# Kernel tuning notes

Hardware: AMD Instinct MI355X
Metric: run time of the kernel (lower is better)

Reference implementation:

```python
import jax, jax.numpy as jnp
import numpy as np
from jax import lax

NPRE = 900        # num_proposal_pre (hardcoded in module)
NPOST = 64        # num_proposal init arg
MAXV = 8          # max vertices of intersection of two convex quads
NMS_THRESH = 0.85
BN_EPS = 1e-5


def boxes3d_to_bev(b):
    # b: (N,7) = (x,y,z,h,w,l,ry) -> BEV rotated box (x1,y1,x2,y2,ry) on x-z plane
    cu, cv = b[:, 0], b[:, 2]
    half_l, half_w = b[:, 5] * 0.5, b[:, 4] * 0.5
    return jnp.stack([cu - half_l, cv - half_w, cu + half_l, cv + half_w, b[:, 6]], axis=-1)


def rect_corners(bev):
    # bev: (N,5) -> (N,4,2) CCW corners of rotated rect
    cx = (bev[:, 0] + bev[:, 2]) * 0.5
    cy = (bev[:, 1] + bev[:, 3]) * 0.5
    hx = (bev[:, 2] - bev[:, 0]) * 0.5
    hy = (bev[:, 3] - bev[:, 1]) * 0.5
    c, s = jnp.cos(bev[:, 4]), jnp.sin(bev[:, 4])
    lx = jnp.stack([-hx, hx, hx, -hx], -1)   # (N,4)
    ly = jnp.stack([-hy, -hy, hy, hy], -1)
    X = cx[:, None] + c[:, None] * lx - s[:, None] * ly
    Y = cy[:, None] + s[:, None] * lx + c[:, None] * ly
    return jnp.stack([X, Y], -1)


def _clip(poly, cnt, a, b):
    # Sutherland-Hodgman clip of poly (MAXV,2) with cnt valid verts by half-plane
    # left of directed edge a->b (clip quad is CCW).
    n = b - a
    def side(p):
        return n[0] * (p[1] - a[1]) - n[1] * (p[0] - a[0])
    out = jnp.zeros_like(poly)
    ocnt = jnp.int32(0)
    for i in range(MAXV):
        valid = i < cnt
        cur = poly[i]
        nxt = poly[jnp.where(i + 1 < cnt, i + 1, 0)]
        dc, dn = side(cur), side(nxt)
        in_c, in_n = dc >= 0, dn >= 0
        e1 = valid & in_c
        out = jnp.where(e1, out.at[ocnt].set(cur), out)
        ocnt = ocnt + e1.astype(jnp.int32)
        e2 = valid & (in_c != in_n)
        denom = dc - dn
        t = dc / jnp.where(denom == 0, 1.0, denom)
        ip = cur + t * (nxt - cur)
        out = jnp.where(e2, out.at[ocnt].set(ip), out)
        ocnt = ocnt + e2.astype(jnp.int32)
    return out, ocnt


def _pair_inter(ca, cb):
    # intersection area of two convex quads given CCW corners (4,2)
    poly = jnp.concatenate([ca, jnp.zeros((MAXV - 4, 2), ca.dtype)], 0)
    cnt = jnp.int32(4)
    for k in range(4):
        poly, cnt = _clip(poly, cnt, cb[k], cb[(k + 1) % 4])
    s = jnp.float32(0.0)
    for i in range(MAXV):
        valid = (i < cnt) & (cnt >= 3)
        j = jnp.where(i + 1 < cnt, i + 1, 0)
        s = s + jnp.where(valid, poly[i, 0] * poly[j, 1] - poly[j, 0] * poly[i, 1], 0.0)
    return jnp.abs(s) * 0.5


def pairwise_iou(corners, areas):
    # row-blocked to keep memory small: lax.map over rows, vmap over cols
    def row(args):
        ci, ai = args
        inter = jax.vmap(lambda cj: _pair_inter(ci, cj))(corners)
        return inter / jnp.maximum(ai + areas - inter, 1e-8)
    return lax.map(row, (corners, areas))


def nms_keep(iou):
    N = iou.shape[0]
    idx = jnp.arange(N)
    def body(i, keep):
        sup = keep[i] & (iou[i] > NMS_THRESH) & (idx > i)
        return keep & (~sup)
    return lax.fori_loop(0, N, body, jnp.ones((N,), bool))


def _forward(search_xyz, search_feature, estimation_cla, template_box,
             W1, b1, gamma, beta, run_mean, run_var, W2, b2):
    B, N = search_xyz.shape[0], search_xyz.shape[1]
    # reg head: conv1d(256->128,k1) + BN(eval) + ReLU + dropout(eval=id) + conv1d(128->4,k1)
    h = jnp.einsum('oi,bin->bon', W1, search_feature) + b1[None, :, None]
    inv = gamma / jnp.sqrt(run_var + BN_EPS)
    h = h * inv[None, :, None] + (beta - run_mean * inv)[None, :, None]
    h = jax.nn.relu(h)
    offset = jnp.einsum('oi,bin->bon', W2, h) + b2[None, :, None]  # (B,4,N)
    offset = jnp.transpose(offset, (0, 2, 1))                       # (B,N,4)
    vote_xyz = search_xyz + offset[..., 0:3]
    tmpl = jnp.broadcast_to(template_box, (B, N, 7))
    proposals = jnp.concatenate([vote_xyz, tmpl[..., 3:6], offset[..., 3:4]], -1)  # (B,N,7)
    scores = jax.nn.sigmoid(estimation_cla[..., 0])  # (B,N)

    def per_batch(sc, pr):
        order = jnp.argsort(-sc)
        s = sc[order[:NPRE]]
        p = pr[order[:NPRE]]
        bev = boxes3d_to_bev(p)
        corners = rect_corners(bev)
        areas = (bev[:, 2] - bev[:, 0]) * (bev[:, 3] - bev[:, 1])
        iou = pairwise_iou(lax.stop_gradient(corners), lax.stop_gradient(areas))
        keep = nms_keep(iou)
        rank = jnp.cumsum(keep.astype(jnp.int32)) - 1
        tgt = jnp.where(keep & (rank < NPOST), rank, NPOST)  # NPOST = dummy slot
        out_b = jnp.zeros((NPOST + 1, 7), p.dtype).at[tgt].set(p)[:NPOST]
        out_s = jnp.zeros((NPOST + 1,), s.dtype).at[tgt].set(s)[:NPOST]
        return out_b, out_s

    ret_bbox3d, ret_scores = jax.vmap(per_batch)(scores, proposals)
    center_xyzs = ret_bbox3d[..., 0:3]
    prop_out = jnp.take(proposals, jnp.array([0, 1, 2, 6]), axis=-1)
    return ret_bbox3d, ret_scores, prop_out, center_xyzs


def setup_inputs():
    key = jax.random.key(0)
    ks = jax.random.split(key, 8)
    B, N, C, H = 8, 16384, 256, 128
    search_xyz = jax.random.normal(ks[0], (B, N, 3), jnp.float32) * 2.0
    search_feature = jax.random.normal(ks[1], (B, C, N), jnp.float32)
    estimation_cla = jax.random.normal(ks[2], (B, N, 1), jnp.float32)
    center = jax.random.normal(ks[3], (B, 1, 3), jnp.float32)
    dims = jax.random.uniform(ks[4], (B, 1, 3), jnp.float32, 1.0, 3.0)
    ry = jax.random.uniform(ks[5], (B, 1, 1), jnp.float32, -np.pi, np.pi)
    template_box = jnp.concatenate([center, dims, ry], -1)
    W1 = jax.random.normal(ks[6], (H, C), jnp.float32) * (1.0 / np.sqrt(C))
    b1 = jnp.zeros((H,), jnp.float32)
    gamma = jnp.ones((H,), jnp.float32)
    beta = jnp.zeros((H,), jnp.float32)
    run_mean = jnp.zeros((H,), jnp.float32)
    run_var = jnp.ones((H,), jnp.float32)
    W2 = jax.random.normal(ks[7], (4, H), jnp.float32) * (1.0 / np.sqrt(H))
    b2 = jnp.zeros((4,), jnp.float32)
    return dict(search_xyz=search_xyz, search_feature=search_feature,
                estimation_cla=estimation_cla, template_box=template_box,
                W1=W1, b1=b1, gamma=gamma, beta=beta,
                run_mean=run_mean, run_var=run_var, W2=W2, b2=b2)


def reference(search_xyz, search_feature, estimation_cla, template_box,
              W1, b1, gamma, beta, run_mean, run_var, W2, b2):
    return _forward(search_xyz, search_feature, estimation_cla, template_box,
                    W1, b1, gamma, beta, run_mean, run_var, W2, b2)
```

## Files before the change

kernel.cpp:

```cpp
#include <hip/hip_runtime.h>
#include <cmath>

#define NTOT 16384
#define NBATCH 8
#define NPRE 900
#define NPOST 64

__global__ __launch_bounds__(256) void mlp_kernel(
    const float* __restrict__ feat, const float* __restrict__ xyz,
    const float* __restrict__ W1, const float* __restrict__ b1,
    const float* __restrict__ gamma, const float* __restrict__ beta,
    const float* __restrict__ rmean, const float* __restrict__ rvar,
    const float* __restrict__ W2, const float* __restrict__ b2,
    float* __restrict__ prop) {
  __shared__ float As[64][128];
  __shared__ float Bs[64][128];
  const int b  = blockIdx.y;
  const int n0 = blockIdx.x * 128;
  const int tid = threadIdx.x;
  const int tr = tid >> 4, tc = tid & 15;
  const float* fb = feat + (size_t)b * 256 * NTOT;

  float acc[8][8];
#pragma unroll
  for (int r = 0; r < 8; ++r)
#pragma unroll
    for (int c = 0; c < 8; ++c) acc[r][c] = 0.f;

  for (int kt = 0; kt < 4; ++kt) {
    {
      const int m = tid & 127, qh = tid >> 7;
#pragma unroll
      for (int p = 0; p < 8; ++p) {
        const int q = qh + p * 2;
        const float4 w = *(const float4*)(W1 + (size_t)m * 256 + kt * 64 + q * 4);
        As[q * 4 + 0][m] = w.x; As[q * 4 + 1][m] = w.y;
        As[q * 4 + 2][m] = w.z; As[q * 4 + 3][m] = w.w;
      }
      const int qq = tid & 31, r0 = tid >> 5;
#pragma unroll
      for (int p = 0; p < 8; ++p) {
        const int k = r0 + p * 8;
        *(float4*)(&Bs[k][qq * 4]) =
            *(const float4*)(fb + (size_t)(kt * 64 + k) * NTOT + n0 + qq * 4);
      }
    }
    __syncthreads();
#pragma unroll 8
    for (int k = 0; k < 64; ++k) {
      float a[8], bb[8];
      *(float4*)&a[0]  = *(const float4*)&As[k][tr * 8];
      *(float4*)&a[4]  = *(const float4*)&As[k][tr * 8 + 4];
      *(float4*)&bb[0] = *(const float4*)&Bs[k][tc * 4];
      *(float4*)&bb[4] = *(const float4*)&Bs[k][64 + tc * 4];
#pragma unroll
      for (int r = 0; r < 8; ++r)
#pragma unroll
        for (int c = 0; c < 8; ++c) acc[r][c] = fmaf(a[r], bb[c], acc[r][c]);
    }
    __syncthreads();
  }

  float po[4][8];
#pragma unroll
  for (int kk = 0; kk < 4; ++kk)
#pragma unroll
    for (int c = 0; c < 8; ++c) po[kk][c] = 0.f;
#pragma unroll
  for (int r = 0; r < 8; ++r) {
    const int row = tr * 8 + r;
    const float inv = gamma[row] / sqrtf(rvar[row] + 1e-5f);
    const float sh  = beta[row] - rmean[row] * inv;
    const float bb1 = b1[row];
    float w2v[4];
#pragma unroll
    for (int kk = 0; kk < 4; ++kk) w2v[kk] = W2[kk * 128 + row];
#pragma unroll
    for (int c = 0; c < 8; ++c) {
      float h = (acc[r][c] + bb1) * inv + sh;
      h = fmaxf(h, 0.f);
#pragma unroll
      for (int kk = 0; kk < 4; ++kk) po[kk][c] += w2v[kk] * h;
    }
  }
  float* po_lds = &As[0][0];
#pragma unroll
  for (int kk = 0; kk < 4; ++kk)
#pragma unroll
    for (int c = 0; c < 8; ++c) {
      const int col = (c < 4) ? (tc * 4 + c) : (64 + tc * 4 + (c - 4));
      po_lds[((tr * 4 + kk) * 128) + col] = po[kk][c];
    }
  __syncthreads();
  float* off_lds = &Bs[0][0];
#pragma unroll
  for (int it = 0; it < 2; ++it) {
    const int idx = tid + it * 256;
    const int kk = idx >> 7, col = idx & 127;
    float sum = b2[kk];
#pragma unroll
    for (int t2 = 0; t2 < 16; ++t2) sum += po_lds[((t2 * 4 + kk) * 128) + col];
    off_lds[kk * 128 + col] = sum;
  }
  __syncthreads();
  if (tid < 128) {
    const int n = n0 + tid;
    const float* sx = xyz + ((size_t)b * NTOT + n) * 3;
    float4 o;
    o.x = sx[0] + off_lds[0 * 128 + tid];
    o.y = sx[1] + off_lds[1 * 128 + tid];
    o.z = sx[2] + off_lds[2 * 128 + tid];
    o.w = off_lds[3 * 128 + tid];
    *(float4*)(prop + ((size_t)b * NTOT + n) * 4) = o;
  }
}

__device__ __forceinline__ float polyclip_reg(
    float s0x, float s0y, float s1x, float s1y,
    float s2x, float s2y, float s3x, float s3y,
    const float cjx[4], const float cjy[4]) {
#pragma clang fp contract(off)
  float vx[8], vy[8];
  vx[0] = s0x; vy[0] = s0y; vx[1] = s1x; vy[1] = s1y;
  vx[2] = s2x; vy[2] = s2y; vx[3] = s3x; vy[3] = s3y;
#pragma unroll
  for (int v = 4; v < 8; ++v) { vx[v] = 0.f; vy[v] = 0.f; }
  int cnt = 4;
#pragma unroll
  for (int e = 0; e < 4; ++e) {
    const float ax = cjx[e], ay = cjy[e];
    const float bx = cjx[(e + 1) & 3], by = cjy[(e + 1) & 3];
    const float nx = bx - ax, ny = by - ay;
    float d[8];
#pragma unroll
    for (int v = 0; v < 8; ++v) d[v] = nx * (vy[v] - ay) - ny * (vx[v] - ax);
    float ox[8], oy[8];
#pragma unroll
    for (int v = 0; v < 8; ++v) { ox[v] = 0.f; oy[v] = 0.f; }
    int oc = 0;
#pragma unroll
    for (int v = 0; v < 8; ++v) {
      const bool valid = v < cnt;
      float nvx, nvy, dn;
      if (v == 7) {
        const bool big = cnt > 8;
        nvx = big ? vx[7] : vx[0]; nvy = big ? vy[7] : vy[0]; dn = big ? d[7] : d[0];
      } else {
        const bool wrap = (v + 1 >= cnt);
        nvx = wrap ? vx[0] : vx[v + 1];
        nvy = wrap ? vy[0] : vy[v + 1];
        dn  = wrap ? d[0]  : d[v + 1];
      }
      const float dc = d[v];
      const bool inc = dc >= 0.f, inn = dn >= 0.f;
      const bool e1 = valid && inc;
#pragma unroll
      for (int s2 = 0; s2 < 8; ++s2) {
        const bool w_ = e1 && (oc == s2);
        ox[s2] = w_ ? vx[v] : ox[s2];
        oy[s2] = w_ ? vy[v] : oy[s2];
      }
      oc += e1 ? 1 : 0;
      const bool e2 = valid && (inc != inn);
      const float den = dc - dn;
      const float t = dc / ((den == 0.f) ? 1.0f : den);
      const float ipx = vx[v] + t * (nvx - vx[v]);
      const float ipy = vy[v] + t * (nvy - vy[v]);
#pragma unroll
      for (int s2 = 0; s2 < 8; ++s2) {
        const bool w_ = e2 && (oc == s2);
        ox[s2] = w_ ? ipx : ox[s2];
        oy[s2] = w_ ? ipy : oy[s2];
      }
      oc += e2 ? 1 : 0;
    }
#pragma unroll
    for (int v = 0; v < 8; ++v) { vx[v] = ox[v]; vy[v] = oy[v]; }
    cnt = oc;
  }
  float s = 0.f;
#pragma unroll
  for (int v = 0; v < 8; ++v) {
    const bool valid = (v < cnt) && (cnt >= 3);
    float jx, jy;
    if (v == 7) {
      const bool big = cnt > 8;
      jx = big ? vx[7] : vx[0]; jy = big ? vy[7] : vy[0];
    } else {
      const bool wrap = (v + 1 >= cnt);
      jx = wrap ? vx[0] : vx[v + 1]; jy = wrap ? vy[0] : vy[v + 1];
    }
    s += valid ? (vx[v] * jy - jx * vy[v]) : 0.f;
  }
  return fabsf(s) * 0.5f;
}

__device__ __forceinline__ bool pair_suppressed(
    const float* __restrict__ corners, const float* __restrict__ areas,
    int b, int i, int j) {
  const float* ci = corners + ((size_t)b * NPRE + i) * 8;
  const float* cj = corners + ((size_t)b * NPRE + j) * 8;
  float cjx[4], cjy[4];
#pragma unroll
  for (int q = 0; q < 4; ++q) { cjx[q] = cj[2 * q]; cjy[q] = cj[2 * q + 1]; }
  const float inter = polyclip_reg(ci[0], ci[1], ci[2], ci[3],
                                   ci[4], ci[5], ci[6], ci[7], cjx, cjy);
  const float ai = areas[(size_t)b * NPRE + i];
  const float aj = areas[(size_t)b * NPRE + j];
  const float iou = inter / fmaxf(ai + aj - inter, 1e-8f);
  return iou > 0.85f;
}

__global__ __launch_bounds__(1024) void select_kernel(
    const float* __restrict__ cla, const float* __restrict__ prop,
    const float* __restrict__ tmpl, float* __restrict__ selbox,
    float* __restrict__ corners, float* __restrict__ areas,
    float* __restrict__ aabb, int* __restrict__ wlcnt) {
  __shared__ unsigned red[17];
  __shared__ int cnt_lds;
  __shared__ unsigned long long cand[1024];
  const int b = blockIdx.x, tid = threadIdx.x;
  if (tid == 0) wlcnt[b] = 0;
  unsigned key[16];
#pragma unroll
  for (int q = 0; q < 16; ++q) {
    const float x = cla[(size_t)b * NTOT + q * 1024 + tid];
    key[q] = __float_as_uint(1.0f / (1.0f + expf(-x)));
  }
  unsigned lo = 0u, hi = 0xFFFFFFFFu;
  unsigned T = 0u;
  bool done = false;
  while (!done && (hi - lo > 1u)) {
    const unsigned mid = lo + ((hi - lo) >> 1);
    int c = 0;
#pragma unroll
    for (int q = 0; q < 16; ++q) c += (key[q] >= mid) ? 1 : 0;
#pragma unroll
    for (int off = 32; off > 0; off >>= 1) c += __shfl_down(c, off);
    __syncthreads();
    if ((tid & 63) == 0) red[tid >> 6] = (unsigned)c;
    __syncthreads();
    if (tid == 0) {
      unsigned s = 0;
      for (int w2 = 0; w2 < 16; ++w2) s += red[w2];
      red[16] = s;
    }
    __syncthreads();
    const unsigned cntv = red[16];
    if (cntv >= NPRE && cntv <= 1024) { T = mid; done = true; }
    else if (cntv >= NPRE) lo = mid;
    else hi = mid;
  }
  if (!done) T = lo;
  if (tid == 0) cnt_lds = 0;
  cand[tid] = 0ull;
  __syncthreads();
#pragma unroll
  for (int q = 0; q < 16; ++q) {
    if (key[q] >= T) {
      const int pos = atomicAdd(&cnt_lds, 1);
      if (pos < 1024)
        cand[pos] = ((unsigned long long)key[q] << 32) |
                    (unsigned long long)(0xFFFFFFFFu - (unsigned)(q * 1024 + tid));
    }
  }
  __syncthreads();
  for (int k = 2; k <= 1024; k <<= 1) {
    for (int j = k >> 1; j > 0; j >>= 1) {
      if (tid < 512) {
        const int i = ((tid & ~(j - 1)) << 1) | (tid & (j - 1));
        const int l = i | j;
        const unsigned long long Pi = cand[i], Pl = cand[l];
        const bool asc = (i & k) == 0;
        if ((Pi < Pl) == asc) { cand[i] = Pl; cand[l] = Pi; }
      }
      __syncthreads();
    }
  }
  if (tid < NPRE) {
    const unsigned long long p = cand[tid];
    const int idx = (int)(0xFFFFFFFFu - (unsigned)(p & 0xFFFFFFFFull));
    const float score = __uint_as_float((unsigned)(p >> 32));
    const float4 pv = *(const float4*)(prop + ((size_t)b * NTOT + idx) * 4);
    const float d3 = tmpl[b * 7 + 3], d4 = tmpl[b * 7 + 4], d5 = tmpl[b * 7 + 5];
    const size_t o8 = ((size_t)b * NPRE + tid) * 8;
    selbox[o8 + 0] = pv.x; selbox[o8 + 1] = pv.y; selbox[o8 + 2] = pv.z;
    selbox[o8 + 3] = d3;   selbox[o8 + 4] = d4;   selbox[o8 + 5] = d5;
    selbox[o8 + 6] = pv.w; selbox[o8 + 7] = score;
    {
#pragma clang fp contract(off)
      const float cu = pv.x, cv = pv.z;
      const float hl = d5 * 0.5f, hw = d4 * 0.5f;
      const float x1 = cu - hl, y1 = cv - hw, x2 = cu + hl, y2 = cv + hw;
      const float cx = (x1 + x2) * 0.5f, cy = (y1 + y2) * 0.5f;
      const float hx = (x2 - x1) * 0.5f, hy = (y2 - y1) * 0.5f;
      const float cr = cosf(pv.w), sr = sinf(pv.w);
      const float lx[4] = {-hx, hx, hx, -hx};
      const float ly[4] = {-hy, -hy, hy, hy};
      float bx0 = 1e30f, by0 = 1e30f, bx1 = -1e30f, by1 = -1e30f;
#pragma unroll
      for (int q = 0; q < 4; ++q) {
        const float X = cx + cr * lx[q] - sr * ly[q];
        const float Y = cy + sr * lx[q] + cr * ly[q];
        corners[o8 + 2 * q]     = X;
        corners[o8 + 2 * q + 1] = Y;
        bx0 = fminf(bx0, X); by0 = fminf(by0, Y);
        bx1 = fmaxf(bx1, X); by1 = fmaxf(by1, Y);
      }
      areas[(size_t)b * NPRE + tid] = (x2 - x1) * (y2 - y1);
      float4 bb; bb.x = bx0; bb.y = by0; bb.z = bx1; bb.w = by1;
      *(float4*)(aabb + ((size_t)b * NPRE + tid) * 4) = bb;
    }
  }
}

__global__ __launch_bounds__(256) void pairgen_kernel(
    const float* __restrict__ aabb, const float* __restrict__ areas,
    const float* __restrict__ corners, unsigned long long* __restrict__ sup,
    unsigned* __restrict__ wl, int* __restrict__ wlcnt, int cap) {
  __shared__ int wsum[4];
  __shared__ int base_s;
  const int i = blockIdx.x, b = blockIdx.y, tid = threadIdx.x;
  if (tid < 16) sup[((size_t)b * NPRE + i) * 16 + tid] = 0ull;
  const float4 bi = *(const float4*)(aabb + ((size_t)b * NPRE + i) * 4);
  const float ai = areas[(size_t)b * NPRE + i];
  bool pass[4];
  int pc = 0;
#pragma unroll
  for (int c = 0; c < 4; ++c) {
    const int j = c * 256 + tid;
    bool p = false;
    if (j > i && j < NPRE) {
      const float4 bj = *(const float4*)(aabb + ((size_t)b * NPRE + j) * 4);
      const float aj = areas[(size_t)b * NPRE + j];
      const float ow = fminf(bi.z, bj.z) - fmaxf(bi.x, bj.x);
      const float oh = fminf(bi.w, bj.w) - fmaxf(bi.y, bj.y);
      const float ov = fmaxf(ow, 0.f) * fmaxf(oh, 0.f);
      p = (ov >= 0.45f * (ai + aj));
    }
    pass[c] = p;
    pc += p ? 1 : 0;
  }
  int inc = pc;
#pragma unroll
  for (int d2 = 1; d2 < 64; d2 <<= 1) {
    const int u = __shfl_up(inc, d2);
    if ((tid & 63) >= d2) inc += u;
  }
  if ((tid & 63) == 63) wsum[tid >> 6] = inc;
  __syncthreads();
  if (tid == 0) {
    const int tot = wsum[0] + wsum[1] + wsum[2] + wsum[3];
    base_s = (tot > 0) ? atomicAdd(&wlcnt[b], tot) : 0;
  }
  __syncthreads();
  int wbase = 0;
#pragma unroll
  for (int w = 0; w < 4; ++w)
    if (w < (tid >> 6)) wbase += wsum[w];
  int myoff = base_s + wbase + (inc - pc);
#pragma unroll
  for (int c = 0; c < 4; ++c) {
    if (pass[c]) {
      const int j = c * 256 + tid;
      const int pos = myoff++;
      if (pos < cap) {
        wl[(size_t)b * cap + pos] = (unsigned)((i << 10) | j);
      } else {
        if (pair_suppressed(corners, areas, b, i, j))
          atomicOr(&sup[((size_t)b * NPRE + i) * 16 + (j >> 6)],
                   1ull << (j & 63));
      }
    }
  }
}

__global__ __launch_bounds__(256) void clip_kernel(
    const float* __restrict__ corners, const float* __restrict__ areas,
    const unsigned* __restrict__ wl, const int* __restrict__ wlcnt, int cap,
    unsigned long long* __restrict__ sup) {
  const int b = blockIdx.y, tid = threadIdx.x;
  const int n = min(wlcnt[b], cap);
  for (int idx = blockIdx.x * 256 + tid; idx < n; idx += gridDim.x * 256) {
    const unsigned e = wl[(size_t)b * cap + idx];
    const int i = (int)(e >> 10), j = (int)(e & 1023u);
    if (pair_suppressed(corners, areas, b, i, j))
      atomicOr(&sup[((size_t)b * NPRE + i) * 16 + (j >> 6)], 1ull << (j & 63));
  }
}

#define NMS_ROWS 904
__global__ __launch_bounds__(1024) void nms_kernel(
    const unsigned long long* __restrict__ sup,
    unsigned long long* __restrict__ keepw) {
  extern __shared__ unsigned long long rows[];
  const int b = blockIdx.x, tid = threadIdx.x;
  const unsigned long long* srow = sup + (size_t)b * NPRE * 16;
  for (int q = tid; q < NMS_ROWS * 16; q += 1024)
    rows[q] = (q < NPRE * 16) ? srow[q] : 0ull;
  __syncthreads();
  if (tid < 64) {
    const int lane = tid;
    const bool ld = lane < 16;
    unsigned long long kw = 0ull;
    if (lane < 14) kw = ~0ull;
    else if (lane == 14) kw = 0xFull;
    unsigned long long r0 = ld ? rows[0 * 16 + lane] : 0ull;
    unsigned long long r1 = ld ? rows[1 * 16 + lane] : 0ull;
    unsigned long long r2 = ld ? rows[2 * 16 + lane] : 0ull;
    unsigned long long r3 = ld ? rows[3 * 16 + lane] : 0ull;
#define NMS_STEP(ii, bufv)                                            \
    {                                                                 \
      const unsigned long long w = __shfl(kw, (ii) >> 6);             \
      if ((w >> ((ii) & 63)) & 1ull) kw &= ~(bufv);                   \
      bufv = ld ? rows[((ii) + 4) * 16 + lane] : 0ull;                \
    }
    for (int i = 0; i < NPRE; i += 4) {
      NMS_STEP(i + 0, r0)
      NMS_STEP(i + 1, r1)
      NMS_STEP(i + 2, r2)
      NMS_STEP(i + 3, r3)
    }
#undef NMS_STEP
    if (lane < 15) keepw[b * 16 + lane] = kw;
  }
}

__global__ __launch_bounds__(128) void out_kernel(
    const float* __restrict__ selbox,
    const unsigned long long* __restrict__ keepw, float* __restrict__ out) {
  const int b = blockIdx.x, t = threadIdx.x;
  float* retb = out + (size_t)b * (NPOST * 7);
  float* rets = out + (size_t)NBATCH * NPOST * 7 + (size_t)b * NPOST;
  float* cent = out + (size_t)NBATCH * NPOST * 7 + (size_t)NBATCH * NPOST +
                (size_t)NBATCH * NTOT * 4 + (size_t)b * (NPOST * 3);
  for (int q = t; q < NPOST * 7; q += 128) retb[q] = 0.f;
  if (t < NPOST) rets[t] = 0.f;
  for (int q = t; q < NPOST * 3; q += 128) cent[q] = 0.f;
  __syncthreads();
  if (t < 64) {
    const unsigned long long kws = (t < 15) ? keepw[b * 16 + t] : 0ull;
    const int pc = __popcll(kws);
    int inc = pc;
    for (int d2 = 1; d2 < 64; d2 <<= 1) {
      const int up = __shfl_up(inc, d2);
      if (t >= d2) inc += up;
    }
    const int ex = inc - pc;
    for (int it = 0; it < 15; ++it) {
      const int i = t + it * 64;
      const int w = (i >> 6) & 63;
      const unsigned long long kword = __shfl(kws, w);
      const int exw = __shfl(ex, w);
      if (i < NPRE) {
        const int bp = i & 63;
        if ((kword >> bp) & 1ull) {
          const int rank =
              exw + __popcll(kword & (((unsigned long long)1 << bp) - 1ull));
          if (rank < NPOST) {
            const float* sb = selbox + ((size_t)b * NPRE + i) * 8;
#pragma unroll
            for (int c = 0; c < 7; ++c) retb[rank * 7 + c] = sb[c];
            rets[rank] = sb[7];
            cent[rank * 3 + 0] = sb[0];
            cent[rank * 3 + 1] = sb[1];
            cent[rank * 3 + 2] = sb[2];
          }
        }
      }
    }
  }
}

extern "C" void kernel_launch(void* const* d_in, const int* in_sizes, int n_in,
                              void* d_out, int out_size, void* d_ws, size_t ws_size,
                              hipStream_t stream) {
  const float* xyz   = (const float*)d_in[0];
  const float* feat  = (const float*)d_in[1];
  const float* cla   = (const float*)d_in[2];
  const float* tmpl  = (const float*)d_in[3];
  const float* W1    = (const float*)d_in[4];
  const float* b1    = (const float*)d_in[5];
  const float* gamma = (const float*)d_in[6];
  const float* beta  = (const float*)d_in[7];
  const float* rmean = (const float*)d_in[8];
  const float* rvar  = (const float*)d_in[9];
  const float* W2    = (const float*)d_in[10];
  const float* b2    = (const float*)d_in[11];
  float* out  = (float*)d_out;
  float* prop = out + (size_t)NBATCH * NPOST * 7 + (size_t)NBATCH * NPOST;

  char* ws = (char*)d_ws;
  float* selbox  = (float*)(ws);
  float* corners = (float*)(ws + 230400);
  float* areas   = (float*)(ws + 460800);
  float* aabb    = (float*)(ws + 489600);
  unsigned long long* sup   = (unsigned long long*)(ws + 604800);
  unsigned long long* keepw = (unsigned long long*)(ws + 1526400);
  int* wlcnt = (int*)(ws + 1527424);
  unsigned* wl = (unsigned*)(ws + 1527456);
  long long avail = (long long)ws_size - 1527456;
  if (avail < 0) avail = 0;
  int cap = (int)(avail / (4 * NBATCH));
  if (cap > 404551) cap = 404551;

  mlp_kernel<<<dim3(NTOT / 128, NBATCH), 256, 0, stream>>>(
      feat, xyz, W1, b1, gamma, beta, rmean, rvar, W2, b2, prop);

  select_kernel<<<NBATCH, 1024, 0, stream>>>(cla, prop, tmpl, selbox, corners,
                                             areas, aabb, wlcnt);

  pairgen_kernel<<<dim3(NPRE, NBATCH), 256, 0, stream>>>(
      aabb, areas, corners, sup, wl, wlcnt, cap);

  clip_kernel<<<dim3(64, NBATCH), 256, 0, stream>>>(corners, areas, wl, wlcnt,
                                                    cap, sup);

  (void)hipFuncSetAttribute((const void*)nms_kernel,
                            hipFuncAttributeMaxDynamicSharedMemorySize,
                            NMS_ROWS * 16 * (int)sizeof(unsigned long long));
  nms_kernel<<<NBATCH, 1024, NMS_ROWS * 16 * sizeof(unsigned long long),
               stream>>>(sup, keepw);

  out_kernel<<<NBATCH, 128, 0, stream>>>(selbox, keepw, out);
}
```

Before: 477.2 us.

## Double-buffer MLP GEMM with async global-to-LDS loads and wider tiles

The first-layer GEMM in mlp_kernel is rewritten to use double-buffered LDS with the global_load_lds builtin, so the next K-slice is fetched while the current one is computed. The output tile widens from 128 to 256 points per block, giving 128 accumulators per thread, and the A tile is stored in an XOR-swizzled layout to avoid bank conflicts. It uses 96KB of dynamic shared memory, which lowers occupancy and raises register pressure, and halves the grid, which risks underfilling the GPU.

```diff
diff --git a/kernel.cpp b/kernel.cpp
--- a/kernel.cpp
+++ b/kernel.cpp
@@ -5,6 +5,20 @@
 #define NBATCH 8
 #define NPRE 900
 #define NPOST 64
+
+#if __has_builtin(__builtin_amdgcn_global_load_lds)
+#define HAVE_GLDS 1
+#define GLDS16(g, l)                                                     \
+  __builtin_amdgcn_global_load_lds(                                      \
+      (const __attribute__((address_space(1))) void*)(g),                \
+      (__attribute__((address_space(3))) void*)(l), 16, 0, 0)
+#else
+#define HAVE_GLDS 0
+#endif
+
+__device__ __forceinline__ float f4c(const float4& v, int kk) {
+  return kk == 0 ? v.x : kk == 1 ? v.y : kk == 2 ? v.z : v.w;
+}
 
 __global__ __launch_bounds__(256) void mlp_kernel(
     const float* __restrict__ feat, const float* __restrict__ xyz,
@@ -13,59 +27,103 @@
     const float* __restrict__ rmean, const float* __restrict__ rvar,
     const float* __restrict__ W2, const float* __restrict__ b2,
     float* __restrict__ prop) {
-  __shared__ float As[64][128];
-  __shared__ float Bs[64][128];
+  extern __shared__ float4 smem4[];
+  float* smem = (float*)smem4;
   const int b  = blockIdx.y;
-  const int n0 = blockIdx.x * 128;
+  const int n0 = blockIdx.x * 256;
   const int tid = threadIdx.x;
   const int tr = tid >> 4, tc = tid & 15;
+  const int w = tid >> 6, l = tid & 63;
   const float* fb = feat + (size_t)b * 256 * NTOT;
 
-  float acc[8][8];
+  float acc[8][16];
 #pragma unroll
   for (int r = 0; r < 8; ++r)
 #pragma unroll
-    for (int c = 0; c < 8; ++c) acc[r][c] = 0.f;
-
-  for (int kt = 0; kt < 4; ++kt) {
-    {
-      const int m = tid & 127, qh = tid >> 7;
-#pragma unroll
-      for (int p = 0; p < 8; ++p) {
-        const int q = qh + p * 2;
-        const float4 w = *(const float4*)(W1 + (size_t)m * 256 + kt * 64 + q * 4);
-        As[q * 4 + 0][m] = w.x; As[q * 4 + 1][m] = w.y;
-        As[q * 4 + 2][m] = w.z; As[q * 4 + 3][m] = w.w;
-      }
-      const int qq = tid & 31, r0 = tid >> 5;
-#pragma unroll
-      for (int p = 0; p < 8; ++p) {
-        const int k = r0 + p * 8;
-        *(float4*)(&Bs[k][qq * 4]) =
-            *(const float4*)(fb + (size_t)(kt * 64 + k) * NTOT + n0 + qq * 4);
-      }
-    }
+    for (int c = 0; c < 16; ++c) acc[r][c] = 0.f;
+
+#if !HAVE_GLDS
+  float4 rA[4], rB[8];
+#endif
+
+#define A_SRC(kt_, q_)                                                    \
+  (W1 + (size_t)(w * 32 + (q_) * 8 + (l >> 3)) * 256 + (kt_) * 32 +       \
+   (((l & 7) ^ (((w * 32 + (q_) * 8 + (l >> 3)) >> 3) & 7)) * 4))
+#define A_DST(buf_, q_) (smem + (size_t)(buf_) * 4096 + (w * 32 + (q_) * 8) * 8 * 4)
+#define B_SRC(kt_, q_) (fb + (size_t)((kt_) * 32 + w * 8 + (q_)) * NTOT + n0 + l * 4)
+#define B_DST(buf_, q_) (smem + 8192 + (size_t)(buf_) * 8192 + (w * 8 + (q_)) * 256)
+
+#if HAVE_GLDS
+#pragma unroll
+  for (int q = 0; q < 4; ++q) GLDS16(A_SRC(0, q), A_DST(0, q));
+#pragma unroll
+  for (int q = 0; q < 8; ++q) GLDS16(B_SRC(0, q), B_DST(0, q));
+#else
+#pragma unroll
+  for (int q = 0; q < 4; ++q) rA[q] = *(const float4*)A_SRC(0, q);
+#pragma unroll
+  for (int q = 0; q < 8; ++q) rB[q] = *(const float4*)B_SRC(0, q);
+#pragma unroll
+  for (int q = 0; q < 4; ++q) *(float4*)(A_DST(0, q) + l * 4) = rA[q];
+#pragma unroll
+  for (int q = 0; q < 8; ++q) *(float4*)(B_DST(0, q) + l * 4) = rB[q];
+#endif
+  __syncthreads();
+
+  for (int kt = 0; kt < 8; ++kt) {
+    const int buf = kt & 1;
+    if (kt + 1 < 8) {
+#if HAVE_GLDS
+#pragma unroll
+      for (int q = 0; q < 4; ++q) GLDS16(A_SRC(kt + 1, q), A_DST(buf ^ 1, q));
+#pragma unroll
+      for (int q = 0; q < 8; ++q) GLDS16(B_SRC(kt + 1, q), B_DST(buf ^ 1, q));
+#else
+#pragma unroll
+      for (int q = 0; q < 4; ++q) rA[q] = *(const float4*)A_SRC(kt + 1, q);
+#pragma unroll
+      for (int q = 0; q < 8; ++q) rB[q] = *(const float4*)B_SRC(kt + 1, q);
+#endif
+    }
+    const float* Asb = smem + (size_t)buf * 4096;
+    const float* Bsb = smem + 8192 + (size_t)buf * 8192;
+    for (int k4 = 0; k4 < 8; ++k4) {
+      float4 a4[8];
+#pragma unroll
+      for (int r = 0; r < 8; ++r)
+        a4[r] = *(const float4*)(Asb + ((tr * 8 + r) * 8 + (k4 ^ (tr & 7))) * 4);
+#pragma unroll
+      for (int kk = 0; kk < 4; ++kk) {
+        const int k = k4 * 4 + kk;
+        float bb[16];
+        *(float4*)&bb[0]  = *(const float4*)(Bsb + k * 256 + tc * 4);
+        *(float4*)&bb[4]  = *(const float4*)(Bsb + k * 256 + 64 + tc * 4);
+        *(float4*)&bb[8]  = *(const float4*)(Bsb + k * 256 + 128 + tc * 4);
+        *(float4*)&bb[12] = *(const float4*)(Bsb + k * 256 + 192 + tc * 4);
+#pragma unroll
+        for (int r = 0; r < 8; ++r) {
+          const float av = f4c(a4[r], kk);
+#pragma unroll
+          for (int c = 0; c < 16; ++c) acc[r][c] = fmaf(av, bb[c], acc[r][c]);
+        }
+      }
+    }
+#if !HAVE_GLDS
+    if (kt + 1 < 8) {
+#pragma unroll
+      for (int q = 0; q < 4; ++q) *(float4*)(A_DST(buf ^ 1, q) + l * 4) = rA[q];
+#pragma unroll
+      for (int q = 0; q < 8; ++q) *(float4*)(B_DST(buf ^ 1, q) + l * 4) = rB[q];
+    }
+#endif
     __syncthreads();
-#pragma unroll 8
-    for (int k = 0; k < 64; ++k) {
-      float a[8], bb[8];
-      *(float4*)&a[0]  = *(const float4*)&As[k][tr * 8];
-      *(float4*)&a[4]  = *(const float4*)&As[k][tr * 8 + 4];
-      *(float4*)&bb[0] = *(const float4*)&Bs[k][tc * 4];
-      *(float4*)&bb[4] = *(const float4*)&Bs[k][64 + tc * 4];
-#pragma unroll
-      for (int r = 0; r < 8; ++r)
-#pragma unroll
-        for (int c = 0; c < 8; ++c) acc[r][c] = fmaf(a[r], bb[c], acc[r][c]);
-    }
-    __syncthreads();
-  }
-
-  float po[4][8];
+  }
+
+  float po[4][16];
 #pragma unroll
   for (int kk = 0; kk < 4; ++kk)
 #pragma unroll
-    for (int c = 0; c < 8; ++c) po[kk][c] = 0.f;
+    for (int c = 0; c < 16; ++c) po[kk][c] = 0.f;
 #pragma unroll
   for (int r = 0; r < 8; ++r) {
     const int row = tr * 8 + r;
@@ -76,43 +134,47 @@
 #pragma unroll
     for (int kk = 0; kk < 4; ++kk) w2v[kk] = W2[kk * 128 + row];
 #pragma unroll
-    for (int c = 0; c < 8; ++c) {
+    for (int c = 0; c < 16; ++c) {
       float h = (acc[r][c] + bb1) * inv + sh;
       h = fmaxf(h, 0.f);
 #pragma unroll
       for (int kk = 0; kk < 4; ++kk) po[kk][c] += w2v[kk] * h;
     }
   }
-  float* po_lds = &As[0][0];
+  float* po_lds = smem;
 #pragma unroll
   for (int kk = 0; kk < 4; ++kk)
 #pragma unroll
-    for (int c = 0; c < 8; ++c) {
-      const int col = (c < 4) ? (tc * 4 + c) : (64 + tc * 4 + (c - 4));
-      po_lds[((tr * 4 + kk) * 128) + col] = po[kk][c];
-    }
-  __syncthreads();
-  float* off_lds = &Bs[0][0];
-#pragma unroll
-  for (int it = 0; it < 2; ++it) {
+    for (int c = 0; c < 16; ++c) {
+      const int col = (c >> 2) * 64 + tc * 4 + (c & 3);
+      po_lds[((tr * 4 + kk) * 256) + col] = po[kk][c];
+    }
+  __syncthreads();
+  float* off_lds = smem + 16384;
+#pragma unroll
+  for (int it = 0; it < 4; ++it) {
     const int idx = tid + it * 256;
-    const int kk = idx >> 7, col = idx & 127;
+    const int kk = idx >> 8, col = idx & 255;
     float sum = b2[kk];
 #pragma unroll
-    for (int t2 = 0; t2 < 16; ++t2) sum += po_lds[((t2 * 4 + kk) * 128) + col];
-    off_lds[kk * 128 + col] = sum;
-  }
-  __syncthreads();
-  if (tid < 128) {
+    for (int t2 = 0; t2 < 16; ++t2) sum += po_lds[((t2 * 4 + kk) * 256) + col];
+    off_lds[kk * 256 + col] = sum;
+  }
+  __syncthreads();
+  {
     const int n = n0 + tid;
     const float* sx = xyz + ((size_t)b * NTOT + n) * 3;
     float4 o;
-    o.x = sx[0] + off_lds[0 * 128 + tid];
-    o.y = sx[1] + off_lds[1 * 128 + tid];
-    o.z = sx[2] + off_lds[2 * 128 + tid];
-    o.w = off_lds[3 * 128 + tid];
+    o.x = sx[0] + off_lds[0 * 256 + tid];
+    o.y = sx[1] + off_lds[1 * 256 + tid];
+    o.z = sx[2] + off_lds[2 * 256 + tid];
+    o.w = off_lds[3 * 256 + tid];
     *(float4*)(prop + ((size_t)b * NTOT + n) * 4) = o;
   }
+#undef A_SRC
+#undef A_DST
+#undef B_SRC
+#undef B_DST
 }
 
 __device__ __forceinline__ float polyclip_reg(
@@ -504,7 +566,9 @@
   int cap = (int)(avail / (4 * NBATCH));
   if (cap > 404551) cap = 404551;
 
-  mlp_kernel<<<dim3(NTOT / 128, NBATCH), 256, 0, stream>>>(
+  (void)hipFuncSetAttribute((const void*)mlp_kernel,
+                            hipFuncAttributeMaxDynamicSharedMemorySize, 98304);
+  mlp_kernel<<<dim3(NTOT / 256, NBATCH), 256, 98304, stream>>>(
       feat, xyz, W1, b1, gamma, beta, rmean, rvar, W2, b2, prop);
 
   select_kernel<<<NBATCH, 1024, 0, stream>>>(cla, prop, tmpl, selbox, corners,
```

Result: slower. 488.0 us (+2.3%).
